# Kernel tuning notes

Measured on AMD Instinct MI355X. Metric: run time of the kernel, lower is better.

Reference implementation:

```python
import jax, jax.numpy as jnp
import numpy as np

D_MODEL = 1024
NUM_HEADS = 16
HEAD_DIM = D_MODEL // NUM_HEADS
SCALE = 1.0 / float(np.sqrt(HEAD_DIM))


def setup_inputs() -> dict:
    key = jax.random.key(0)
    ks = jax.random.split(key, 9)
    B, S, D = 2, 2048, D_MODEL
    # Xavier-uniform bound for square (D, D) linear layers
    bound = float(np.sqrt(6.0 / (D + D)))
    def xavier(k):
        return jax.random.uniform(k, (D, D), jnp.float32, -bound, bound)
    return {
        "x": jax.random.normal(ks[0], (B, S, D), jnp.float32),
        "Wq": xavier(ks[1]), "bq": jnp.zeros((D,), jnp.float32),
        "Wk": xavier(ks[2]), "bk": jnp.zeros((D,), jnp.float32),
        "Wv": xavier(ks[3]), "bv": jnp.zeros((D,), jnp.float32),
        "Wo": xavier(ks[4]), "bo": jnp.zeros((D,), jnp.float32),
    }


def reference(x, Wq, bq, Wk, bk, Wv, bv, Wo, bo):
    B, S, D = x.shape
    H, Hd = NUM_HEADS, HEAD_DIM
    # torch Linear: y = x @ W.T + b
    def proj(W, b):
        y = jnp.einsum("bsd,ed->bse", x, W) + b
        return y.reshape(B, S, H, Hd).transpose(0, 2, 1, 3)  # (B,H,S,Hd)
    Q = proj(Wq, bq)
    K = proj(Wk, bk)
    V = proj(Wv, bv)
    # scaled scores (B,H,S,S) + additive causal mask (0 / -inf)
    scores = jnp.einsum("bhqd,bhkd->bhqk", Q, K) * SCALE
    causal = jnp.where(
        jnp.tril(jnp.ones((S, S), dtype=bool)), 0.0, -jnp.inf
    ).astype(scores.dtype)
    scores = scores + causal
    attn = jax.nn.softmax(scores, axis=-1)
    attn = jnp.nan_to_num(attn, nan=0.0)  # no-op here (causal rows never fully masked)
    # dropout p=0.0 -> identity
    ctx = jnp.einsum("bhqk,bhkd->bhqd", attn, V)  # (B,H,S,Hd)
    ctx = ctx.transpose(0, 2, 1, 3).reshape(B, S, D)
    out = jnp.einsum("bsd,ed->bse", ctx, Wo) + bo
    return out, attn
```

## Files before the change

### kernel.cpp

```cpp
#include <hip/hip_runtime.h>

typedef unsigned short u16;
using short8 = __attribute__((ext_vector_type(8))) short;
using f32x4  = __attribute__((ext_vector_type(4))) float;
using u16x4  = __attribute__((ext_vector_type(4))) unsigned short;

__device__ __forceinline__ u16 f2bf(float f) {
  union { float f; unsigned int u; } v; v.f = f;
  unsigned int u = v.u + 0x7FFFu + ((v.u >> 16) & 1u);
  return (u16)(u >> 16);
}
__device__ __forceinline__ float bf2f(u16 u) {
  union { unsigned int u; float f; } v; v.u = ((unsigned int)u) << 16;
  return v.f;
}
__device__ __forceinline__ void glds16(const void* g, void* l) {
  __builtin_amdgcn_global_load_lds(
      (const __attribute__((address_space(1))) void*)g,
      (__attribute__((address_space(3))) void*)l, 16, 0, 0);
}

__global__ __launch_bounds__(256) void cast_all(
    const float* __restrict__ x, const float* __restrict__ wq,
    const float* __restrict__ wk, const float* __restrict__ wv,
    const float* __restrict__ wo,
    u16* __restrict__ xb, u16* __restrict__ wqb, u16* __restrict__ wkb,
    u16* __restrict__ wvb, u16* __restrict__ wob) {
  int i = blockIdx.x * 256 + threadIdx.x;
  const float4* src; ushort4* dst; int off;
  if (i < 1048576)      { src = (const float4*)x;  dst = (ushort4*)xb;  off = i; }
  else if (i < 1310720) { src = (const float4*)wq; dst = (ushort4*)wqb; off = i - 1048576; }
  else if (i < 1572864) { src = (const float4*)wk; dst = (ushort4*)wkb; off = i - 1310720; }
  else if (i < 1835008) { src = (const float4*)wv; dst = (ushort4*)wvb; off = i - 1572864; }
  else                  { src = (const float4*)wo; dst = (ushort4*)wob; off = i - 1835008; }
  float4 v = src[off];
  ushort4 o;
  o.x = f2bf(v.x); o.y = f2bf(v.y); o.z = f2bf(v.z); o.w = f2bf(v.w);
  dst[off] = o;
}

template<int OUT_F32>
__global__ __launch_bounds__(256) void gemm_nt_glds(
    const u16* __restrict__ A,
    const u16* __restrict__ B0, const u16* __restrict__ B1, const u16* __restrict__ B2,
    const float* __restrict__ bias0, const float* __restrict__ bias1, const float* __restrict__ bias2,
    void* __restrict__ C0, void* __restrict__ C1, void* __restrict__ C2,
    int K)
{
  __shared__ u16 As[128 * 64];
  __shared__ u16 Bs[128 * 64];
  const int bn = blockIdx.x, bm = blockIdx.y;
  const int sel = bn >> 3, bnl = bn & 7;
  const u16* B = sel == 0 ? B0 : (sel == 1 ? B1 : B2);
  const float* bias = sel == 0 ? bias0 : (sel == 1 ? bias1 : bias2);
  void* C = sel == 0 ? C0 : (sel == 1 ? C1 : C2);

  const int tid = threadIdx.x;
  const int w = tid >> 6, lane = tid & 63, quad = lane >> 4, l16 = lane & 15;
  const int wm = w >> 1, wn = w & 1;
  const int srow = lane >> 3, gc = (lane & 7) ^ srow;

  const u16* aseg = A + (size_t)(bm * 128 + w * 32 + srow) * K + gc * 8;
  const u16* bseg = B + (size_t)(bnl * 128 + w * 32 + srow) * K + gc * 8;

  const f32x4 z4 = {0.f, 0.f, 0.f, 0.f};
  f32x4 acc[4][4];
#pragma unroll
  for (int mt = 0; mt < 4; mt++)
#pragma unroll
    for (int nt = 0; nt < 4; nt++) acc[mt][nt] = z4;

  for (int k0 = 0; k0 < K; k0 += 64) {
    __syncthreads();
#pragma unroll
    for (int j = 0; j < 4; j++) {
      glds16(aseg + (size_t)(j * 8) * K + k0, (u16*)As + (w * 4 + j) * 512);
      glds16(bseg + (size_t)(j * 8) * K + k0, (u16*)Bs + (w * 4 + j) * 512);
    }
    __syncthreads();
#pragma unroll
    for (int ks = 0; ks < 2; ks++) {
      short8 af[4], bf[4];
#pragma unroll
      for (int mt = 0; mt < 4; mt++) {
        int row = wm * 64 + mt * 16 + l16;
        int chk = (ks * 4 + quad) ^ (row & 7);
        af[mt] = *(const short8*)((const short*)As + row * 64 + chk * 8);
      }
#pragma unroll
      for (int nt = 0; nt < 4; nt++) {
        int row = wn * 64 + nt * 16 + l16;
        int chk = (ks * 4 + quad) ^ (row & 7);
        bf[nt] = *(const short8*)((const short*)Bs + row * 64 + chk * 8);
      }
#pragma unroll
      for (int mt = 0; mt < 4; mt++)
#pragma unroll
        for (int nt = 0; nt < 4; nt++)
          acc[mt][nt] = __builtin_amdgcn_mfma_f32_16x16x32_bf16(af[mt], bf[nt], acc[mt][nt], 0, 0, 0);
    }
  }
#pragma unroll
  for (int mt = 0; mt < 4; mt++) {
    int row0 = bm * 128 + wm * 64 + mt * 16 + quad * 4;
#pragma unroll
    for (int nt = 0; nt < 4; nt++) {
      int col = bnl * 128 + wn * 64 + nt * 16 + l16;
      float bv = bias[col];
#pragma unroll
      for (int r = 0; r < 4; r++) {
        float v = acc[mt][nt][r] + bv;
        if (OUT_F32) ((float*)C)[(size_t)(row0 + r) * 1024 + col] = v;
        else         ((u16*)C)[(size_t)(row0 + r) * 1024 + col] = f2bf(v);
      }
    }
  }
}

__global__ __launch_bounds__(256) void transpose_bf16(const u16* __restrict__ in,
                                                      u16* __restrict__ out) {
  __shared__ u16 t[64][65];
  const int ct = blockIdx.x, rt = blockIdx.y, b = blockIdx.z;
  const u16* ip = in + (size_t)b * 2048 * 1024;
  u16* op = out + (size_t)b * 2048 * 1024;
#pragma unroll
  for (int i = 0; i < 16; i++) {
    int idx = threadIdx.x + i * 256; int r = idx >> 6, c = idx & 63;
    t[r][c] = ip[(size_t)(rt * 64 + r) * 1024 + ct * 64 + c];
  }
  __syncthreads();
#pragma unroll
  for (int i = 0; i < 16; i++) {
    int idx = threadIdx.x + i * 256; int r = idx >> 6, c = idx & 63;
    op[(size_t)(ct * 64 + r) * 2048 + rt * 64 + c] = t[c][r];
  }
}

__global__ __launch_bounds__(256) void attn_kernel(
    const u16* __restrict__ Qb, const u16* __restrict__ Kbuf,
    const u16* __restrict__ Vtb, float* __restrict__ attn,
    u16* __restrict__ ctx)
{
  __shared__ u16 Qs[128 * 64];
  __shared__ u16 KVs[128 * 64];
  __shared__ u16 Ps[128 * 128];
  __shared__ float ls[128];
  __shared__ float rls[128];

  const int flat = blockIdx.x;
  const int half = flat >> 8, r0 = flat & 255;
  const int bh = (half << 4) | (r0 >> 4);
  const int qb = half ? (15 - (r0 & 15)) : (r0 & 15);
  const int b = bh >> 4, h = bh & 15;

  const int tid = threadIdx.x;
  const int w = tid >> 6, lane = tid & 63, quad = lane >> 4, l16 = lane & 15;
  const int wm = w >> 1, wn = w & 1;
  const int srow8 = lane >> 3, gc8 = (lane & 7) ^ srow8;
  const int srow16 = lane >> 4, sc16 = lane & 15;

  const int S = 2048, D = 1024;
  const u16* Qg = Qb + ((size_t)b * S + qb * 128) * D + h * 64;
  const u16* Kg = Kbuf + (size_t)b * S * D + h * 64;
  const u16* Vg = Vtb + ((size_t)b * D + h * 64) * S;
  float* attng = attn + ((size_t)(b * 16 + h) * S + qb * 128) * S;

  const float SCALE = 0.125f;
  const f32x4 z4 = {0.f, 0.f, 0.f, 0.f};

#pragma unroll
  for (int j = 0; j < 4; j++)
    glds16(Qg + (size_t)(w * 32 + j * 8 + srow8) * D + gc8 * 8, (u16*)Qs + (w * 4 + j) * 512);
  if (tid < 128) ls[tid] = 0.f;

  for (int kb = 0; kb <= qb; kb++) {
    __syncthreads();
#pragma unroll
    for (int j = 0; j < 4; j++)
      glds16(Kg + (size_t)(kb * 128 + w * 32 + j * 8 + srow8) * D + gc8 * 8,
             (u16*)KVs + (w * 4 + j) * 512);
    __syncthreads();
    f32x4 acc[4][4];
#pragma unroll
    for (int mt = 0; mt < 4; mt++)
#pragma unroll
      for (int nt = 0; nt < 4; nt++) acc[mt][nt] = z4;
#pragma unroll
    for (int ks = 0; ks < 2; ks++) {
      short8 af[4], bf[4];
#pragma unroll
      for (int mt = 0; mt < 4; mt++) {
        int row = wm * 64 + mt * 16 + l16;
        int chk = (ks * 4 + quad) ^ (row & 7);
        af[mt] = *(const short8*)((const short*)Qs + row * 64 + chk * 8);
      }
#pragma unroll
      for (int nt = 0; nt < 4; nt++) {
        int row = wn * 64 + nt * 16 + l16;
        int chk = (ks * 4 + quad) ^ (row & 7);
        bf[nt] = *(const short8*)((const short*)KVs + row * 64 + chk * 8);
      }
#pragma unroll
      for (int mt = 0; mt < 4; mt++)
#pragma unroll
        for (int nt = 0; nt < 4; nt++)
          acc[mt][nt] = __builtin_amdgcn_mfma_f32_16x16x32_bf16(af[mt], bf[nt], acc[mt][nt], 0, 0, 0);
    }
#pragma unroll
    for (int mt = 0; mt < 4; mt++) {
#pragma unroll
      for (int rr = 0; rr < 4; rr++) {
        int row_local = wm * 64 + mt * 16 + quad * 4 + rr;
        int gq = qb * 128 + row_local;
        float psum = 0.f;
#pragma unroll
        for (int nt = 0; nt < 4; nt++) {
          int gk = kb * 128 + wn * 64 + nt * 16 + l16;
          float v = acc[mt][nt][rr] * SCALE;
          psum += (gk <= gq) ? __expf(fminf(v, 30.f)) : 0.f;
        }
        psum += __shfl_xor(psum, 1);
        psum += __shfl_xor(psum, 2);
        psum += __shfl_xor(psum, 4);
        psum += __shfl_xor(psum, 8);
        if (l16 == 0) atomicAdd(&ls[row_local], psum);
      }
    }
  }
  __syncthreads();
  if (tid < 128) rls[tid] = 1.0f / ls[tid];

  f32x4 cacc[2][4];
#pragma unroll
  for (int mt = 0; mt < 2; mt++)
#pragma unroll
    for (int nt = 0; nt < 4; nt++) cacc[mt][nt] = z4;

  for (int kb = 0; kb <= qb; kb++) {
    __syncthreads();
#pragma unroll
    for (int j = 0; j < 4; j++)
      glds16(Kg + (size_t)(kb * 128 + w * 32 + j * 8 + srow8) * D + gc8 * 8,
             (u16*)KVs + (w * 4 + j) * 512);
    __syncthreads();
    f32x4 acc[4][4];
#pragma unroll
    for (int mt = 0; mt < 4; mt++)
#pragma unroll
      for (int nt = 0; nt < 4; nt++) acc[mt][nt] = z4;
#pragma unroll
    for (int ks = 0; ks < 2; ks++) {
      short8 af[4], bf[4];
#pragma unroll
      for (int mt = 0; mt < 4; mt++) {
        int row = wm * 64 + mt * 16 + l16;
        int chk = (ks * 4 + quad) ^ (row & 7);
        af[mt] = *(const short8*)((const short*)Qs + row * 64 + chk * 8);
      }
#pragma unroll
      for (int nt = 0; nt < 4; nt++) {
        int row = wn * 64 + nt * 16 + l16;
        int chk = (ks * 4 + quad) ^ (row & 7);
        bf[nt] = *(const short8*)((const short*)KVs + row * 64 + chk * 8);
      }
#pragma unroll
      for (int mt = 0; mt < 4; mt++)
#pragma unroll
        for (int nt = 0; nt < 4; nt++)
          acc[mt][nt] = __builtin_amdgcn_mfma_f32_16x16x32_bf16(af[mt], bf[nt], acc[mt][nt], 0, 0, 0);
    }
#pragma unroll
    for (int mt = 0; mt < 4; mt++) {
#pragma unroll
      for (int rr = 0; rr < 4; rr++) {
        int row_local = wm * 64 + mt * 16 + quad * 4 + rr;
        int gq = qb * 128 + row_local;
        float rl = rls[row_local];
#pragma unroll
        for (int nt = 0; nt < 4; nt++) {
          int colk = wn * 64 + nt * 16 + l16;
          int gk = kb * 128 + colk;
          float v = acc[mt][nt][rr] * SCALE;
          float p = (gk <= gq) ? __expf(fminf(v, 30.f)) * rl : 0.f;
          Ps[row_local * 128 + (((colk >> 3) ^ (row_local & 7)) << 3) + (colk & 7)] = f2bf(p);
        }
      }
    }
    __syncthreads();
#pragma unroll
    for (int j = 0; j < 4; j++) {
      int r0v = (w * 4 + j) * 4;
      int row = r0v + srow16;
      int gcv = sc16 ^ (row & 7);
      glds16(Vg + (size_t)row * S + kb * 128 + gcv * 8, (u16*)KVs + r0v * 128);
    }
#pragma unroll
    for (int s = 0; s < 16; s++) {
      int e4 = s * 256 + tid;
      int row = e4 >> 5, col = (e4 & 31) * 4;
      int chunk = (col >> 3) ^ (row & 7);
      u16x4 pv = *(const u16x4*)((const u16*)Ps + row * 128 + chunk * 8 + (col & 7));
      f32x4 o;
      o[0] = bf2f(pv[0]); o[1] = bf2f(pv[1]); o[2] = bf2f(pv[2]); o[3] = bf2f(pv[3]);
      __builtin_nontemporal_store(o, (f32x4*)(attng + (size_t)row * S + kb * 128 + col));
    }
    __syncthreads();
#pragma unroll
    for (int ks = 0; ks < 4; ks++) {
      short8 pf[2], vf[4];
#pragma unroll
      for (int mt = 0; mt < 2; mt++) {
        int row = w * 32 + mt * 16 + l16;
        int chk = (ks * 4 + quad) ^ (row & 7);
        pf[mt] = *(const short8*)((const short*)Ps + row * 128 + chk * 8);
      }
#pragma unroll
      for (int nt = 0; nt < 4; nt++) {
        int row = nt * 16 + l16;
        int chk = (ks * 4 + quad) ^ (row & 7);
        vf[nt] = *(const short8*)((const short*)KVs + row * 128 + chk * 8);
      }
#pragma unroll
      for (int mt = 0; mt < 2; mt++)
#pragma unroll
        for (int nt = 0; nt < 4; nt++)
          cacc[mt][nt] = __builtin_amdgcn_mfma_f32_16x16x32_bf16(pf[mt], vf[nt], cacc[mt][nt], 0, 0, 0);
    }
  }

  {
    int kstart = (qb + 1) * 128;
    const f32x4 zz = {0.f, 0.f, 0.f, 0.f};
    for (int rr = 0; rr < 128; rr++) {
      float* rowp = attng + (size_t)rr * S;
      for (int c = kstart + tid * 4; c < S; c += 1024)
        __builtin_nontemporal_store(zz, (f32x4*)(rowp + c));
    }
  }

#pragma unroll
  for (int mt = 0; mt < 2; mt++)
#pragma unroll
    for (int nt = 0; nt < 4; nt++)
#pragma unroll
      for (int rr = 0; rr < 4; rr++) {
        int row_local = w * 32 + mt * 16 + quad * 4 + rr;
        int col = nt * 16 + l16;
        ctx[((size_t)b * S + qb * 128 + row_local) * D + h * 64 + col] = f2bf(cacc[mt][nt][rr]);
      }
}

extern "C" void kernel_launch(void* const* d_in, const int* in_sizes, int n_in,
                              void* d_out, int out_size, void* d_ws, size_t ws_size,
                              hipStream_t stream) {
  const float* x  = (const float*)d_in[0];
  const float* Wq = (const float*)d_in[1];
  const float* bq = (const float*)d_in[2];
  const float* Wk = (const float*)d_in[3];
  const float* bk = (const float*)d_in[4];
  const float* Wv = (const float*)d_in[5];
  const float* bv = (const float*)d_in[6];
  const float* Wo = (const float*)d_in[7];
  const float* bo = (const float*)d_in[8];

  float* out_f32  = (float*)d_out;
  float* attn_out = (float*)d_out + 4194304;

  char* w = (char*)d_ws;
  u16* xb   = (u16*)(w + 0);
  u16* Wqb  = (u16*)(w + 8388608);
  u16* Wkb  = (u16*)(w + 10485760);
  u16* Wvb  = (u16*)(w + 12582912);
  u16* Wob  = (u16*)(w + 14680064);
  u16* Qbuf = (u16*)(w + 16777216);
  u16* Kbuf = (u16*)(w + 25165824);
  u16* Vbuf = (u16*)(w + 33554432);
  u16* Vtb  = (u16*)(w + 41943040);
  u16* ctxb = (u16*)(w + 50331648);

  cast_all<<<8192, 256, 0, stream>>>(x, Wq, Wk, Wv, Wo, xb, Wqb, Wkb, Wvb, Wob);

  gemm_nt_glds<0><<<dim3(24, 32), 256, 0, stream>>>(
      xb, Wqb, Wkb, Wvb, bq, bk, bv, Qbuf, Kbuf, Vbuf, 1024);

  transpose_bf16<<<dim3(16, 32, 2), 256, 0, stream>>>(Vbuf, Vtb);

  attn_kernel<<<512, 256, 0, stream>>>(Qbuf, Kbuf, Vtb, attn_out, ctxb);

  gemm_nt_glds<1><<<dim3(8, 32), 256, 0, stream>>>(
      ctxb, Wob, Wob, Wob, bo, bo, bo, out_f32, out_f32, out_f32, 1024);
}
```

Measured before the change: 802.3 us.

## Fuse V transpose into QKV GEMM, fold scale into Q, double-buffer K in attention

The QKV GEMM epilogue now writes V already transposed through an LDS staging tile, which removes the separate transpose kernel and its extra round trip through global memory. The softmax scale is folded into Q at projection time. The attention kernel keeps Q fragments in registers and double-buffers K tiles so the next load overlaps the current MFMA work. It accumulates row sums in registers with one reduction at the end instead of LDS atomics on every tile, and uses s_setprio around MFMA sections. The price is higher register pressure, and rounding Q to bf16 after scaling by 0.125 is exact because it is a power of two.

```diff
diff --git a/kernel.cpp b/kernel.cpp
--- a/kernel.cpp
+++ b/kernel.cpp
@@ -39,7 +39,7 @@
   dst[off] = o;
 }
 
-template<int OUT_F32>
+template<int MODE>
 __global__ __launch_bounds__(256) void gemm_nt_glds(
     const u16* __restrict__ A,
     const u16* __restrict__ B0, const u16* __restrict__ B1, const u16* __restrict__ B2,
@@ -47,8 +47,9 @@
     void* __restrict__ C0, void* __restrict__ C1, void* __restrict__ C2,
     int K)
 {
-  __shared__ u16 As[128 * 64];
-  __shared__ u16 Bs[128 * 64];
+  __shared__ u16 smem[16896];
+  u16* As = smem;
+  u16* Bs = smem + 8192;
   const int bn = blockIdx.x, bm = blockIdx.y;
   const int sel = bn >> 3, bnl = bn & 7;
   const u16* B = sel == 0 ? B0 : (sel == 1 ? B1 : B2);
@@ -74,8 +75,8 @@
     __syncthreads();
 #pragma unroll
     for (int j = 0; j < 4; j++) {
-      glds16(aseg + (size_t)(j * 8) * K + k0, (u16*)As + (w * 4 + j) * 512);
-      glds16(bseg + (size_t)(j * 8) * K + k0, (u16*)Bs + (w * 4 + j) * 512);
+      glds16(aseg + (size_t)(j * 8) * K + k0, As + (w * 4 + j) * 512);
+      glds16(bseg + (size_t)(j * 8) * K + k0, Bs + (w * 4 + j) * 512);
     }
     __syncthreads();
 #pragma unroll
@@ -100,39 +101,50 @@
           acc[mt][nt] = __builtin_amdgcn_mfma_f32_16x16x32_bf16(af[mt], bf[nt], acc[mt][nt], 0, 0, 0);
     }
   }
-#pragma unroll
-  for (int mt = 0; mt < 4; mt++) {
-    int row0 = bm * 128 + wm * 64 + mt * 16 + quad * 4;
-#pragma unroll
-    for (int nt = 0; nt < 4; nt++) {
-      int col = bnl * 128 + wn * 64 + nt * 16 + l16;
-      float bv = bias[col];
-#pragma unroll
-      for (int r = 0; r < 4; r++) {
-        float v = acc[mt][nt][r] + bv;
-        if (OUT_F32) ((float*)C)[(size_t)(row0 + r) * 1024 + col] = v;
-        else         ((u16*)C)[(size_t)(row0 + r) * 1024 + col] = f2bf(v);
-      }
-    }
-  }
-}
-
-__global__ __launch_bounds__(256) void transpose_bf16(const u16* __restrict__ in,
-                                                      u16* __restrict__ out) {
-  __shared__ u16 t[64][65];
-  const int ct = blockIdx.x, rt = blockIdx.y, b = blockIdx.z;
-  const u16* ip = in + (size_t)b * 2048 * 1024;
-  u16* op = out + (size_t)b * 2048 * 1024;
-#pragma unroll
-  for (int i = 0; i < 16; i++) {
-    int idx = threadIdx.x + i * 256; int r = idx >> 6, c = idx & 63;
-    t[r][c] = ip[(size_t)(rt * 64 + r) * 1024 + ct * 64 + c];
-  }
-  __syncthreads();
-#pragma unroll
-  for (int i = 0; i < 16; i++) {
-    int idx = threadIdx.x + i * 256; int r = idx >> 6, c = idx & 63;
-    op[(size_t)(ct * 64 + r) * 2048 + rt * 64 + c] = t[c][r];
+
+  if (MODE == 0 && sel == 2) {
+    __syncthreads();
+#pragma unroll
+    for (int mt = 0; mt < 4; mt++) {
+      int r0 = wm * 64 + mt * 16 + quad * 4;
+#pragma unroll
+      for (int nt = 0; nt < 4; nt++) {
+        int c = wn * 64 + nt * 16 + l16;
+        float bvv = bias[bnl * 128 + c];
+        u16x4 pk;
+#pragma unroll
+        for (int r = 0; r < 4; r++) pk[r] = f2bf(acc[mt][nt][r] + bvv);
+        *(u16x4*)(smem + c * 132 + r0) = pk;
+      }
+    }
+    __syncthreads();
+    const int bb = bm >> 4;
+    const size_t sb = (size_t)(bm & 15) * 128;
+    u16* Cv = (u16*)C;
+#pragma unroll
+    for (int i = 0; i < 16; i++) {
+      int idx = tid + i * 256;
+      int dr = idx >> 5, c4 = (idx & 31) * 4;
+      u16x4 v = *(const u16x4*)(smem + dr * 132 + c4);
+      *(u16x4*)(Cv + ((size_t)bb * 1024 + bnl * 128 + dr) * 2048 + sb + c4) = v;
+    }
+  } else {
+    const float cmul = (MODE == 0 && sel == 0) ? 0.125f : 1.0f;
+#pragma unroll
+    for (int mt = 0; mt < 4; mt++) {
+      int row0 = bm * 128 + wm * 64 + mt * 16 + quad * 4;
+#pragma unroll
+      for (int nt = 0; nt < 4; nt++) {
+        int col = bnl * 128 + wn * 64 + nt * 16 + l16;
+        float bv = bias[col];
+#pragma unroll
+        for (int r = 0; r < 4; r++) {
+          float v = (acc[mt][nt][r] + bv) * cmul;
+          if (MODE) ((float*)C)[(size_t)(row0 + r) * 1024 + col] = v;
+          else      ((u16*)C)[(size_t)(row0 + r) * 1024 + col] = f2bf(v);
+        }
+      }
+    }
   }
 }
 
@@ -141,11 +153,9 @@
     const u16* __restrict__ Vtb, float* __restrict__ attn,
     u16* __restrict__ ctx)
 {
-  __shared__ u16 Qs[128 * 64];
-  __shared__ u16 KVs[128 * 64];
+  __shared__ u16 Ks[2][128 * 64];
   __shared__ u16 Ps[128 * 128];
   __shared__ float ls[128];
-  __shared__ float rls[128];
 
   const int flat = blockIdx.x;
   const int half = flat >> 8, r0 = flat & 255;
@@ -165,70 +175,115 @@
   const u16* Vg = Vtb + ((size_t)b * D + h * 64) * S;
   float* attng = attn + ((size_t)(b * 16 + h) * S + qb * 128) * S;
 
-  const float SCALE = 0.125f;
   const f32x4 z4 = {0.f, 0.f, 0.f, 0.f};
 
 #pragma unroll
   for (int j = 0; j < 4; j++)
-    glds16(Qg + (size_t)(w * 32 + j * 8 + srow8) * D + gc8 * 8, (u16*)Qs + (w * 4 + j) * 512);
+    glds16(Qg + (size_t)(w * 32 + j * 8 + srow8) * D + gc8 * 8, (u16*)Ps + (w * 4 + j) * 512);
   if (tid < 128) ls[tid] = 0.f;
+#pragma unroll
+  for (int j = 0; j < 4; j++)
+    glds16(Kg + (size_t)(w * 32 + j * 8 + srow8) * D + gc8 * 8, Ks[0] + (w * 4 + j) * 512);
+  __syncthreads();
+
+  short8 qf[4][2];
+#pragma unroll
+  for (int mt = 0; mt < 4; mt++) {
+    int row = wm * 64 + mt * 16 + l16;
+#pragma unroll
+    for (int ks = 0; ks < 2; ks++) {
+      int chk = (ks * 4 + quad) ^ (row & 7);
+      qf[mt][ks] = *(const short8*)((const short*)Ps + row * 64 + chk * 8);
+    }
+  }
+
+  float rowsum[4][4];
+#pragma unroll
+  for (int mt = 0; mt < 4; mt++)
+#pragma unroll
+    for (int rr = 0; rr < 4; rr++) rowsum[mt][rr] = 0.f;
 
   for (int kb = 0; kb <= qb; kb++) {
-    __syncthreads();
-#pragma unroll
-    for (int j = 0; j < 4; j++)
-      glds16(Kg + (size_t)(kb * 128 + w * 32 + j * 8 + srow8) * D + gc8 * 8,
-             (u16*)KVs + (w * 4 + j) * 512);
-    __syncthreads();
+    if (kb) __syncthreads();
+    if (kb < qb) {
+#pragma unroll
+      for (int j = 0; j < 4; j++)
+        glds16(Kg + (size_t)((kb + 1) * 128 + w * 32 + j * 8 + srow8) * D + gc8 * 8,
+               Ks[(kb + 1) & 1] + (w * 4 + j) * 512);
+    }
+    const u16* kbf = Ks[kb & 1];
     f32x4 acc[4][4];
 #pragma unroll
     for (int mt = 0; mt < 4; mt++)
 #pragma unroll
       for (int nt = 0; nt < 4; nt++) acc[mt][nt] = z4;
+    __builtin_amdgcn_s_setprio(1);
 #pragma unroll
     for (int ks = 0; ks < 2; ks++) {
-      short8 af[4], bf[4];
-#pragma unroll
-      for (int mt = 0; mt < 4; mt++) {
-        int row = wm * 64 + mt * 16 + l16;
-        int chk = (ks * 4 + quad) ^ (row & 7);
-        af[mt] = *(const short8*)((const short*)Qs + row * 64 + chk * 8);
-      }
+      short8 bf[4];
 #pragma unroll
       for (int nt = 0; nt < 4; nt++) {
         int row = wn * 64 + nt * 16 + l16;
         int chk = (ks * 4 + quad) ^ (row & 7);
-        bf[nt] = *(const short8*)((const short*)KVs + row * 64 + chk * 8);
+        bf[nt] = *(const short8*)((const short*)kbf + row * 64 + chk * 8);
       }
 #pragma unroll
       for (int mt = 0; mt < 4; mt++)
 #pragma unroll
         for (int nt = 0; nt < 4; nt++)
-          acc[mt][nt] = __builtin_amdgcn_mfma_f32_16x16x32_bf16(af[mt], bf[nt], acc[mt][nt], 0, 0, 0);
-    }
-#pragma unroll
-    for (int mt = 0; mt < 4; mt++) {
-#pragma unroll
-      for (int rr = 0; rr < 4; rr++) {
-        int row_local = wm * 64 + mt * 16 + quad * 4 + rr;
-        int gq = qb * 128 + row_local;
-        float psum = 0.f;
-#pragma unroll
-        for (int nt = 0; nt < 4; nt++) {
-          int gk = kb * 128 + wn * 64 + nt * 16 + l16;
-          float v = acc[mt][nt][rr] * SCALE;
-          psum += (gk <= gq) ? __expf(fminf(v, 30.f)) : 0.f;
+          acc[mt][nt] = __builtin_amdgcn_mfma_f32_16x16x32_bf16(qf[mt][ks], bf[nt], acc[mt][nt], 0, 0, 0);
+    }
+    __builtin_amdgcn_s_setprio(0);
+    if (kb < qb) {
+#pragma unroll
+      for (int mt = 0; mt < 4; mt++)
+#pragma unroll
+        for (int rr = 0; rr < 4; rr++) {
+          float s = 0.f;
+#pragma unroll
+          for (int nt = 0; nt < 4; nt++)
+            s += __expf(fminf(acc[mt][nt][rr], 30.f));
+          rowsum[mt][rr] += s;
         }
-        psum += __shfl_xor(psum, 1);
-        psum += __shfl_xor(psum, 2);
-        psum += __shfl_xor(psum, 4);
-        psum += __shfl_xor(psum, 8);
-        if (l16 == 0) atomicAdd(&ls[row_local], psum);
-      }
-    }
-  }
+    } else {
+#pragma unroll
+      for (int mt = 0; mt < 4; mt++)
+#pragma unroll
+        for (int rr = 0; rr < 4; rr++) {
+          int rloc = wm * 64 + mt * 16 + quad * 4 + rr;
+          float s = 0.f;
+#pragma unroll
+          for (int nt = 0; nt < 4; nt++) {
+            int ck = wn * 64 + nt * 16 + l16;
+            s += (ck <= rloc) ? __expf(fminf(acc[mt][nt][rr], 30.f)) : 0.f;
+          }
+          rowsum[mt][rr] += s;
+        }
+    }
+  }
+
+#pragma unroll
+  for (int mt = 0; mt < 4; mt++)
+#pragma unroll
+    for (int rr = 0; rr < 4; rr++) {
+      float s = rowsum[mt][rr];
+      s += __shfl_xor(s, 1);
+      s += __shfl_xor(s, 2);
+      s += __shfl_xor(s, 4);
+      s += __shfl_xor(s, 8);
+      if (l16 == 0) atomicAdd(&ls[wm * 64 + mt * 16 + quad * 4 + rr], s);
+    }
   __syncthreads();
-  if (tid < 128) rls[tid] = 1.0f / ls[tid];
+  float rl[4][4];
+#pragma unroll
+  for (int mt = 0; mt < 4; mt++)
+#pragma unroll
+    for (int rr = 0; rr < 4; rr++)
+      rl[mt][rr] = 1.0f / ls[wm * 64 + mt * 16 + quad * 4 + rr];
+
+#pragma unroll
+  for (int j = 0; j < 4; j++)
+    glds16(Kg + (size_t)(w * 32 + j * 8 + srow8) * D + gc8 * 8, Ks[0] + (w * 4 + j) * 512);
 
   f32x4 cacc[2][4];
 #pragma unroll
@@ -237,62 +292,57 @@
     for (int nt = 0; nt < 4; nt++) cacc[mt][nt] = z4;
 
   for (int kb = 0; kb <= qb; kb++) {
-    __syncthreads();
-#pragma unroll
-    for (int j = 0; j < 4; j++)
-      glds16(Kg + (size_t)(kb * 128 + w * 32 + j * 8 + srow8) * D + gc8 * 8,
-             (u16*)KVs + (w * 4 + j) * 512);
-    __syncthreads();
-    f32x4 acc[4][4];
-#pragma unroll
-    for (int mt = 0; mt < 4; mt++)
-#pragma unroll
-      for (int nt = 0; nt < 4; nt++) acc[mt][nt] = z4;
-#pragma unroll
-    for (int ks = 0; ks < 2; ks++) {
-      short8 af[4], bf[4];
-#pragma unroll
-      for (int mt = 0; mt < 4; mt++) {
-        int row = wm * 64 + mt * 16 + l16;
-        int chk = (ks * 4 + quad) ^ (row & 7);
-        af[mt] = *(const short8*)((const short*)Qs + row * 64 + chk * 8);
-      }
-#pragma unroll
-      for (int nt = 0; nt < 4; nt++) {
-        int row = wn * 64 + nt * 16 + l16;
-        int chk = (ks * 4 + quad) ^ (row & 7);
-        bf[nt] = *(const short8*)((const short*)KVs + row * 64 + chk * 8);
-      }
-#pragma unroll
-      for (int mt = 0; mt < 4; mt++)
-#pragma unroll
-        for (int nt = 0; nt < 4; nt++)
-          acc[mt][nt] = __builtin_amdgcn_mfma_f32_16x16x32_bf16(af[mt], bf[nt], acc[mt][nt], 0, 0, 0);
-    }
-#pragma unroll
-    for (int mt = 0; mt < 4; mt++) {
-#pragma unroll
-      for (int rr = 0; rr < 4; rr++) {
-        int row_local = wm * 64 + mt * 16 + quad * 4 + rr;
-        int gq = qb * 128 + row_local;
-        float rl = rls[row_local];
-#pragma unroll
-        for (int nt = 0; nt < 4; nt++) {
-          int colk = wn * 64 + nt * 16 + l16;
-          int gk = kb * 128 + colk;
-          float v = acc[mt][nt][rr] * SCALE;
-          float p = (gk <= gq) ? __expf(fminf(v, 30.f)) * rl : 0.f;
-          Ps[row_local * 128 + (((colk >> 3) ^ (row_local & 7)) << 3) + (colk & 7)] = f2bf(p);
-        }
-      }
-    }
     __syncthreads();
 #pragma unroll
     for (int j = 0; j < 4; j++) {
       int r0v = (w * 4 + j) * 4;
       int row = r0v + srow16;
       int gcv = sc16 ^ (row & 7);
-      glds16(Vg + (size_t)row * S + kb * 128 + gcv * 8, (u16*)KVs + r0v * 128);
+      glds16(Vg + (size_t)row * S + kb * 128 + gcv * 8, Ks[1] + r0v * 128);
+    }
+    f32x4 acc[4][4];
+#pragma unroll
+    for (int mt = 0; mt < 4; mt++)
+#pragma unroll
+      for (int nt = 0; nt < 4; nt++) acc[mt][nt] = z4;
+    __builtin_amdgcn_s_setprio(1);
+#pragma unroll
+    for (int ks = 0; ks < 2; ks++) {
+      short8 bf[4];
+#pragma unroll
+      for (int nt = 0; nt < 4; nt++) {
+        int row = wn * 64 + nt * 16 + l16;
+        int chk = (ks * 4 + quad) ^ (row & 7);
+        bf[nt] = *(const short8*)((const short*)Ks[0] + row * 64 + chk * 8);
+      }
+#pragma unroll
+      for (int mt = 0; mt < 4; mt++)
+#pragma unroll
+        for (int nt = 0; nt < 4; nt++)
+          acc[mt][nt] = __builtin_amdgcn_mfma_f32_16x16x32_bf16(qf[mt][ks], bf[nt], acc[mt][nt], 0, 0, 0);
+    }
+    __builtin_amdgcn_s_setprio(0);
+    bool diag = (kb == qb);
+#pragma unroll
+    for (int mt = 0; mt < 4; mt++)
+#pragma unroll
+      for (int rr = 0; rr < 4; rr++) {
+        int rloc = wm * 64 + mt * 16 + quad * 4 + rr;
+        float rlv = rl[mt][rr];
+#pragma unroll
+        for (int nt = 0; nt < 4; nt++) {
+          int colk = wn * 64 + nt * 16 + l16;
+          float e = __expf(fminf(acc[mt][nt][rr], 30.f)) * rlv;
+          if (diag && colk > rloc) e = 0.f;
+          Ps[rloc * 128 + (((colk >> 3) ^ (rloc & 7)) << 3) + (colk & 7)] = f2bf(e);
+        }
+      }
+    __syncthreads();
+    if (kb < qb) {
+#pragma unroll
+      for (int j = 0; j < 4; j++)
+        glds16(Kg + (size_t)((kb + 1) * 128 + w * 32 + j * 8 + srow8) * D + gc8 * 8,
+               Ks[0] + (w * 4 + j) * 512);
     }
 #pragma unroll
     for (int s = 0; s < 16; s++) {
@@ -304,7 +354,7 @@
       o[0] = bf2f(pv[0]); o[1] = bf2f(pv[1]); o[2] = bf2f(pv[2]); o[3] = bf2f(pv[3]);
       __builtin_nontemporal_store(o, (f32x4*)(attng + (size_t)row * S + kb * 128 + col));
     }
-    __syncthreads();
+    __builtin_amdgcn_s_setprio(1);
 #pragma unroll
     for (int ks = 0; ks < 4; ks++) {
       short8 pf[2], vf[4];
@@ -318,7 +368,7 @@
       for (int nt = 0; nt < 4; nt++) {
         int row = nt * 16 + l16;
         int chk = (ks * 4 + quad) ^ (row & 7);
-        vf[nt] = *(const short8*)((const short*)KVs + row * 128 + chk * 8);
+        vf[nt] = *(const short8*)((const short*)Ks[1] + row * 128 + chk * 8);
       }
 #pragma unroll
       for (int mt = 0; mt < 2; mt++)
@@ -326,6 +376,7 @@
         for (int nt = 0; nt < 4; nt++)
           cacc[mt][nt] = __builtin_amdgcn_mfma_f32_16x16x32_bf16(pf[mt], vf[nt], cacc[mt][nt], 0, 0, 0);
     }
+    __builtin_amdgcn_s_setprio(0);
   }
 
   {
@@ -374,16 +425,13 @@
   u16* Wob  = (u16*)(w + 14680064);
   u16* Qbuf = (u16*)(w + 16777216);
   u16* Kbuf = (u16*)(w + 25165824);
-  u16* Vbuf = (u16*)(w + 33554432);
   u16* Vtb  = (u16*)(w + 41943040);
   u16* ctxb = (u16*)(w + 50331648);
 
   cast_all<<<8192, 256, 0, stream>>>(x, Wq, Wk, Wv, Wo, xb, Wqb, Wkb, Wvb, Wob);
 
   gemm_nt_glds<0><<<dim3(24, 32), 256, 0, stream>>>(
-      xb, Wqb, Wkb, Wvb, bq, bk, bv, Qbuf, Kbuf, Vbuf, 1024);
-
-  transpose_bf16<<<dim3(16, 32, 2), 256, 0, stream>>>(Vbuf, Vtb);
+      xb, Wqb, Wkb, Wvb, bq, bk, bv, Qbuf, Kbuf, Vtb, 1024);
 
   attn_kernel<<<512, 256, 0, stream>>>(Qbuf, Kbuf, Vtb, attn_out, ctxb);
 
```

After: 713.8 us. 1.12x faster.
